# Kernel optimization log

Hardware: AMD Instinct MI355X
Metric: run time of the kernel (lower is better)

Reference implementation:

```python
import jax, jax.numpy as jnp
import numpy as np

B, R, P, DP, DR, N, RK = 4, 256, 64, 384, 512, 48, 24


def _ln(x, w, b, eps=1e-5):
    m = x.mean(-1, keepdims=True)
    v = ((x - m) ** 2).mean(-1, keepdims=True)
    return (x - m) / jnp.sqrt(v + eps) * w + b


def _l2norm(x, eps=1e-6):
    return x / jnp.maximum(jnp.linalg.norm(x, axis=-1, keepdims=True), eps)


def setup_inputs() -> dict:
    key = jax.random.key(0)
    ks = jax.random.split(key, 16)
    s = 0.02
    rnd = lambda k, shp: jax.random.normal(k, shp, jnp.float32) * s
    inp = {
        'patch_tokens': jax.random.normal(ks[0], (B, R, P, DP), jnp.float32),
        'patch_mask': jax.random.randint(ks[1], (B, R, P), 0, 2) > 0,
        'near_mask': jax.random.randint(ks[2], (R, R), 0, 2) > 0,
        'far_mask': jax.random.randint(ks[3], (R, R), 0, 2) > 0,
        'local_pos': rnd(ks[4], (1, 1, P, DP)),
        'gate_ln_w': jnp.ones(DP), 'gate_ln_b': jnp.zeros(DP),
        'gate_w1': rnd(ks[5], (DP, DR)), 'gate_b1': jnp.zeros(DR),
        'gate_w2': rnd(ks[6], (DR, 1)), 'gate_b2': jnp.zeros(1),
        'proj_ln1_w': jnp.ones(DP), 'proj_ln1_b': jnp.zeros(DP),
        'proj_w1': rnd(ks[7], (DP, DR)), 'proj_b1': jnp.zeros(DR),
        'proj_w2': rnd(ks[8], (DR, DR)), 'proj_b2': jnp.zeros(DR),
        'proj_ln2_w': jnp.ones(DR), 'proj_ln2_b': jnp.zeros(DR),
        'in_proj_w': rnd(ks[9], (DR, 2 * DR)),
        'x_proj_w': rnd(ks[10], (DR, RK + 2 * N)),
        'dt_w': rnd(ks[11], (RK, DR)),
        'dt_b': jax.random.uniform(ks[12], (DR,), jnp.float32, -4.0, -2.0),
        'A_log': jnp.tile(jnp.log(jnp.arange(1, N + 1, dtype=jnp.float32))[None, :], (DR, 1)),
        'D_param': jnp.ones(DR),
        'out_proj_w': rnd(ks[13], (DR, DR)),
        'scan_ln_w': jnp.ones(DR), 'scan_ln_b': jnp.zeros(DR),
    }
    return inp


def _forward(patch_tokens, patch_mask, near_mask, far_mask, local_pos,
             gate_ln_w, gate_ln_b, gate_w1, gate_b1, gate_w2, gate_b2,
             proj_ln1_w, proj_ln1_b, proj_w1, proj_b1, proj_w2, proj_b2,
             proj_ln2_w, proj_ln2_b, in_proj_w, x_proj_w, dt_w, dt_b,
             A_log, D_param, out_proj_w, scan_ln_w, scan_ln_b):
    # ---- GatedRegionAggregator ----
    x = patch_tokens + local_pos  # [B,R,P,DP]
    g = _ln(x, gate_ln_w, gate_ln_b)
    g = jax.nn.gelu(g @ gate_w1 + gate_b1, approximate=False)
    logits = (g @ gate_w2 + gate_b2)[..., 0]  # [B,R,P]
    logits = jnp.where(patch_mask, logits, jnp.finfo(logits.dtype).min)
    attn = jax.nn.softmax(logits, axis=-1) * patch_mask
    attn = attn / jnp.maximum(attn.sum(-1, keepdims=True), 1e-6)
    pooled = jnp.einsum('brp,brpd->brd', attn, x)  # [B,R,DP]
    p = _ln(pooled, proj_ln1_w, proj_ln1_b)
    p = jax.nn.gelu(p @ proj_w1 + proj_b1, approximate=False)
    p = _ln(p @ proj_w2 + proj_b2, proj_ln2_w, proj_ln2_b)
    p = jnp.nan_to_num(p, nan=0.0, posinf=1.0, neginf=-1.0)
    region = _l2norm(p)  # [B,R,DR]

    # ---- SlowSelectiveScan1D over region sequence (L = R) ----
    xz = region @ in_proj_w  # [B,L,2*DR]
    u, z = jnp.split(xz, 2, axis=-1)
    prm = u @ x_proj_w  # [B,L,RK+2N]
    dt_raw, Bm, Cm = prm[..., :RK], prm[..., RK:RK + N], prm[..., RK + N:]
    delta = jnp.minimum(jax.nn.softplus(dt_raw @ dt_w + dt_b), 10.0)  # [B,L,DR]
    A = -jnp.minimum(jnp.exp(A_log), 1e4)  # [DR,N]
    dA = jnp.exp(jnp.clip(delta[..., None] * A[None, None], -30.0, 30.0))  # [B,L,DR,N]
    dBu = delta[..., None] * Bm[:, :, None, :] * u[..., None]  # [B,L,DR,N]
    log_cumA = jnp.cumsum(jnp.log(jnp.maximum(dA, 1e-38)), axis=1)
    h = jnp.exp(log_cumA) * jnp.cumsum(dBu * jnp.exp(-log_cumA), axis=1)
    y_seq = jnp.einsum('bln,bldn->bld', Cm, h) + D_param * u
    y = (y_seq * jax.nn.silu(z)) @ out_proj_w
    out = _ln(region + jnp.nan_to_num(y, nan=0.0, posinf=1.0, neginf=-1.0),
              scan_ln_w, scan_ln_b)  # [B,R,DR]

    # ---- topology_loss_static ----
    rt = _l2norm(out.astype(jnp.float32))
    sim = jnp.einsum('brd,bsd->brs', rt, rt)  # [B,R,R]
    near = near_mask.astype(sim.dtype)[None]
    far = far_mask.astype(sim.dtype)[None]
    near_loss = ((1.0 - sim) * near).sum() / jnp.maximum(near.sum(), 1.0)
    far_loss = (jax.nn.relu(sim - 0.2) * far).sum() / jnp.maximum(far.sum(), 1.0)
    return out, near_loss + far_loss


def reference(patch_tokens, patch_mask, near_mask, far_mask, local_pos,
              gate_ln_w, gate_ln_b, gate_w1, gate_b1, gate_w2, gate_b2,
              proj_ln1_w, proj_ln1_b, proj_w1, proj_b1, proj_w2, proj_b2,
              proj_ln2_w, proj_ln2_b, in_proj_w, x_proj_w, dt_w, dt_b,
              A_log, D_param, out_proj_w, scan_ln_w, scan_ln_b):
    return _forward(patch_tokens, patch_mask, near_mask, far_mask, local_pos,
                    gate_ln_w, gate_ln_b, gate_w1, gate_b1, gate_w2, gate_b2,
                    proj_ln1_w, proj_ln1_b, proj_w1, proj_b1, proj_w2, proj_b2,
                    proj_ln2_w, proj_ln2_b, in_proj_w, x_proj_w, dt_w, dt_b,
                    A_log, D_param, out_proj_w, scan_ln_w, scan_ln_b)
```

## Files before the change

### kernel.cpp

```cpp
#include <hip/hip_runtime.h>
#include <hip/hip_bf16.h>
#include <math.h>

#define B_ 4
#define R_ 256
#define P_ 64
#define DP_ 384
#define DR_ 512
#define N_ 48
#define RK_ 24
#define MROWS (B_*R_*P_)
#define REGS  (B_*R_)

typedef unsigned short ushort_t;
typedef __attribute__((ext_vector_type(8))) short bf16x8;
typedef __attribute__((ext_vector_type(4))) float f32x4;

#define GLOAD16(g, l) __builtin_amdgcn_global_load_lds( \
    (const __attribute__((address_space(1))) unsigned int*)(g), \
    (__attribute__((address_space(3))) unsigned int*)(l), 16, 0, 0)

#define OFF_PW1  0
#define OFF_PW2  196608
#define OFF_INPW 458752
#define OFF_XPW  983040
#define OFF_DTW  1044480
#define NW_TOT   1056768

__device__ __forceinline__ float us2f(unsigned short u){
  union { unsigned int i; float f; } x; x.i = ((unsigned int)u) << 16; return x.f;
}
__device__ __forceinline__ unsigned short f2us(float f){
  __hip_bfloat16 h = __float2bfloat16(f);
  return *reinterpret_cast<unsigned short*>(&h);
}
__device__ __forceinline__ float gelu_f(float x){
  return x / (1.0f + __expf(-1.702f * x));
}
__device__ __forceinline__ float wred_sum(float v){
#pragma unroll
  for (int m = 1; m < 64; m <<= 1) v += __shfl_xor(v, m, 64);
  return v;
}
__device__ __forceinline__ void block_sum4(float v[4], float* s){
  int lane = threadIdx.x & 63, wid = threadIdx.x >> 6;
#pragma unroll
  for (int i = 0; i < 4; ++i){
    float x = v[i];
#pragma unroll
    for (int m = 1; m < 64; m <<= 1) x += __shfl_xor(x, m, 64);
    if (lane == 0) s[wid * 4 + i] = x;
  }
  __syncthreads();
  if (threadIdx.x < 4){
    float t = 0.f;
    for (int t2 = 0; t2 < 8; ++t2) t += s[t2 * 4 + threadIdx.x];
    s[32 + threadIdx.x] = t;
  }
  __syncthreads();
#pragma unroll
  for (int i = 0; i < 4; ++i) v[i] = s[32 + i];
  __syncthreads();
}
__device__ __forceinline__ void block_sum2(float& a, float& b, float* s){
  int lane = threadIdx.x & 63, wid = threadIdx.x >> 6;
  float x = a, y = b;
#pragma unroll
  for (int m = 1; m < 64; m <<= 1){ x += __shfl_xor(x, m, 64); y += __shfl_xor(y, m, 64); }
  if (lane == 0){ s[wid * 2] = x; s[wid * 2 + 1] = y; }
  __syncthreads();
  if (threadIdx.x < 2){
    float t = 0.f;
    for (int j = 0; j < 8; ++j) t += s[j * 2 + threadIdx.x];
    s[16 + threadIdx.x] = t;
  }
  __syncthreads();
  a = s[16]; b = s[17];
  __syncthreads();
}

__global__ __launch_bounds__(512) void k_prep(
    const float* __restrict__ gw1, const float* __restrict__ glnw,
    const float* __restrict__ glnb, const float* __restrict__ gb1,
    ushort_t* __restrict__ W1pT, float* __restrict__ s1,
    float* __restrict__ b1p, float* __restrict__ accum){
  __shared__ float pss[8][64], psb[8][64];
  int tid = threadIdx.x, seg = tid >> 6, nl = tid & 63;
  int n = blockIdx.x * 64 + nl;
  if (blockIdx.x == 0 && tid < 4) accum[tid] = 0.f;
  float s = 0.f, sb = 0.f;
  int k0 = seg * 48;
  for (int i = 0; i < 48; ++i){
    int k = k0 + i;
    float w1 = gw1[k * DR_ + n];
    float v = glnw[k] * w1;
    unsigned short vr = f2us(v);
    s  += us2f(vr);
    sb += glnb[k] * w1;
    W1pT[(size_t)n * DP_ + k] = vr;
  }
  pss[seg][nl] = s; psb[seg][nl] = sb;
  __syncthreads();
  if (tid < 64){
    float ts = 0.f, tb = 0.f;
    for (int j = 0; j < 8; ++j){ ts += pss[j][tid]; tb += psb[j][tid]; }
    s1[blockIdx.x * 64 + tid] = ts;
    b1p[blockIdx.x * 64 + tid] = gb1[blockIdx.x * 64 + tid] + tb;
  }
}

__global__ __launch_bounds__(512) void k_cast(
    const float* __restrict__ pw1, const float* __restrict__ pw2,
    const float* __restrict__ inpw, const float* __restrict__ xpw,
    const float* __restrict__ dtw, ushort_t* __restrict__ dst){
  int i = (blockIdx.x * 512 + threadIdx.x) * 4;
  if (i >= NW_TOT) return;
  const float* s; int off;
  if (i < OFF_PW2){ s = pw1; off = OFF_PW1; }
  else if (i < OFF_INPW){ s = pw2; off = OFF_PW2; }
  else if (i < OFF_XPW){ s = inpw; off = OFF_INPW; }
  else if (i < OFF_DTW){ s = xpw; off = OFF_XPW; }
  else { s = dtw; off = OFF_DTW; }
  float4 v = *(const float4*)(s + (i - off));
  ushort_t* d = dst + i;
  d[0] = f2us(v.x); d[1] = f2us(v.y); d[2] = f2us(v.z); d[3] = f2us(v.w);
}

__global__ __launch_bounds__(512) void k_xform(
    const float* __restrict__ pt, const float* __restrict__ lp,
    ushort_t* __restrict__ xb, float* __restrict__ mu, float* __restrict__ rsg){
  int tid = threadIdx.x, w = tid >> 6, lane = tid & 63;
  size_t r = (size_t)blockIdx.x * 8 + w;
  int p = (int)(r & (P_ - 1));
  const float* xr = pt + r * DP_ + lane * 6;
  const float* lr = lp + (size_t)p * DP_ + lane * 6;
  float x[6];
  float s = 0.f, ss = 0.f;
#pragma unroll
  for (int i = 0; i < 6; i += 2){
    float2 a = *(const float2*)(xr + i);
    float2 b = *(const float2*)(lr + i);
    x[i] = a.x + b.x; x[i + 1] = a.y + b.y;
  }
#pragma unroll
  for (int i = 0; i < 6; ++i){ s += x[i]; ss += x[i] * x[i]; }
  s = wred_sum(s); ss = wred_sum(ss);
  if (lane == 0){
    float m = s * (1.f / DP_);
    float var = ss * (1.f / DP_) - m * m;
    mu[r] = m;
    rsg[r] = rsqrtf(var + 1e-5f);
  }
  ushort_t* xw = xb + r * DP_ + lane * 6;
#pragma unroll
  for (int i = 0; i < 6; i += 2){
    ushort2 u2; u2.x = f2us(x[i]); u2.y = f2us(x[i + 1]);
    *(ushort2*)(xw + i) = u2;
  }
}

__global__ __launch_bounds__(1024, 4) void k_gate_pool(
    const ushort_t* __restrict__ xb,
    const ushort_t* __restrict__ BT,
    const float* __restrict__ mu, const float* __restrict__ rsg,
    const float* __restrict__ s1, const float* __restrict__ b1p,
    const float* __restrict__ w2, const int* __restrict__ pmask,
    float* __restrict__ pooled){
  __shared__ __align__(16) ushort_t Abuf[2][128 * 64];
  __shared__ float wpart[16][128];
  __shared__ float logit_lds[128];
  __shared__ float smu[128], srs[128];
  __shared__ float attn2[2][64];
  int tid = threadIdx.x;
  int lane = tid & 63, w = tid >> 6;
  int t = lane & 15, g = lane >> 4;
  long r0 = (long)blockIdx.x * 128;
  if (tid < 128){
    smu[tid] = mu[r0 + tid];
    srs[tid] = rsg[r0 + tid];
  }

  f32x4 acc[8][2];
#pragma unroll
  for (int m = 0; m < 8; ++m)
#pragma unroll
    for (int n = 0; n < 2; ++n) acc[m][n] = (f32x4){0.f, 0.f, 0.f, 0.f};

  int ro = lane >> 3, c = lane & 7;
  int srow = (w << 3) + ro;
  const ushort_t* asrc = xb + (size_t)(r0 + srow) * DP_ + ((c ^ (srow & 7)) << 3);

  GLOAD16(asrc, Abuf[0] + (w << 9));
  __syncthreads();

  for (int kt = 0; kt < 6; ++kt){
    int cb = kt & 1;
    if (kt < 5) GLOAD16(asrc + (kt + 1) * 64, Abuf[cb ^ 1] + (w << 9));
    bf16x8 bfr[2][2];
#pragma unroll
    for (int kk = 0; kk < 2; ++kk)
#pragma unroll
      for (int n = 0; n < 2; ++n){
        int col = w * 32 + n * 16 + t;
        bfr[kk][n] = *(const bf16x8*)(BT + (size_t)col * DP_ + kt * 64 + (kk * 4 + g) * 8);
      }
#pragma unroll
    for (int kk = 0; kk < 2; ++kk){
      int ch = kk * 4 + g;
#pragma unroll
      for (int m = 0; m < 8; ++m){
        int row = m * 16 + t;
        bf16x8 af = *(const bf16x8*)(Abuf[cb] + row * 64 + ((ch ^ (row & 7)) << 3));
#pragma unroll
        for (int n = 0; n < 2; ++n)
          acc[m][n] = __builtin_amdgcn_mfma_f32_16x16x32_bf16(af, bfr[kk][n], acc[m][n], 0, 0, 0);
      }
    }
    __syncthreads();
  }

  float w2c[2], s1c[2], b1c[2];
#pragma unroll
  for (int n = 0; n < 2; ++n){
    int col = w * 32 + n * 16 + t;
    w2c[n] = w2[col]; s1c[n] = s1[col]; b1c[n] = b1p[col];
  }
#pragma unroll
  for (int m = 0; m < 8; ++m){
#pragma unroll
    for (int j = 0; j < 4; ++j){
      int rl = m * 16 + g * 4 + j;
      float mur = smu[rl], rs = srs[rl];
      float part = 0.f;
#pragma unroll
      for (int n = 0; n < 2; ++n){
        float gp = rs * acc[m][n][j] - mur * rs * s1c[n] + b1c[n];
        part += gelu_f(gp) * w2c[n];
      }
#pragma unroll
      for (int msk = 1; msk < 16; msk <<= 1) part += __shfl_xor(part, msk, 16);
      if (t == 0) wpart[w][rl] = part;
    }
  }
  __syncthreads();
  if (tid < 128){
    float s = 0.f;
#pragma unroll
    for (int wi = 0; wi < 16; ++wi) s += wpart[wi][tid];
    logit_lds[tid] = s;
  }
  __syncthreads();

  int half = tid >> 9, lt = tid & 511;
  long rr0 = r0 + half * 64;
  if (lt < 64){
    int mk = pmask[rr0 + lt];
    float lv = logit_lds[half * 64 + lt];
    float lm = mk ? lv : -3.4e38f;
    float M = lm;
#pragma unroll
    for (int m2 = 1; m2 < 64; m2 <<= 1) M = fmaxf(M, __shfl_xor(M, m2, 64));
    float e = mk ? __expf(lv - M) : 0.f;
    float S = e;
#pragma unroll
    for (int m2 = 1; m2 < 64; m2 <<= 1) S += __shfl_xor(S, m2, 64);
    float a = (S > 0.f) ? e / S : 0.f;
    float S2 = a;
#pragma unroll
    for (int m2 = 1; m2 < 64; m2 <<= 1) S2 += __shfl_xor(S2, m2, 64);
    attn2[half][lt] = a / fmaxf(S2, 1e-6f);
  }
  __syncthreads();

  float* pbuf = (float*)Abuf;
  if (lt < 384){
    int pg = lt / 48, cc = lt % 48;
    float a8[8] = {0,0,0,0,0,0,0,0};
#pragma unroll
    for (int i = 0; i < 8; ++i){
      int p = pg + i * 8;
      bf16x8 v = *(const bf16x8*)(xb + (size_t)(rr0 + p) * DP_ + cc * 8);
      float ap = attn2[half][p];
#pragma unroll
      for (int j = 0; j < 8; ++j) a8[j] = fmaf(ap, us2f((unsigned short)v[j]), a8[j]);
    }
#pragma unroll
    for (int j = 0; j < 8; ++j) pbuf[(half * 8 + pg) * DP_ + cc * 8 + j] = a8[j];
  }
  __syncthreads();
  if (lt < 384){
    float s = 0.f;
#pragma unroll
    for (int g2 = 0; g2 < 8; ++g2) s += pbuf[(half * 8 + g2) * DP_ + lt];
    pooled[(long)(2 * blockIdx.x + half) * DP_ + lt] = s;
  }
}

__global__ __launch_bounds__(512, 4) void k_region(
    const float* __restrict__ pooled,
    const float* __restrict__ ln1w, const float* __restrict__ ln1b,
    const ushort_t* __restrict__ wblob, const float* __restrict__ pb1,
    const float* __restrict__ pb2,
    const float* __restrict__ ln2w, const float* __restrict__ ln2b,
    const float* __restrict__ dtb,
    float* __restrict__ region, float* __restrict__ uT, float* __restrict__ zT,
    float* __restrict__ deltaT, float* __restrict__ BmT, float* __restrict__ CmT){
  const ushort_t* pw1b  = wblob + OFF_PW1;
  const ushort_t* pw2b  = wblob + OFF_PW2;
  const ushort_t* inpwb = wblob + OFF_INPW;
  const ushort_t* xpwb  = wblob + OFF_XPW;
  const ushort_t* dtwb  = wblob + OFF_DTW;
  __shared__ __align__(16) float xr[2][DP_];
  __shared__ __align__(16) float p1[2][DR_];
  __shared__ __align__(16) float rg[2][DR_];
  __shared__ __align__(16) float us[2][DR_];
  __shared__ float ps[4][2][128];
  __shared__ float prm[2][RK_ + 2 * N_];
  __shared__ float red[24];
  int tid = threadIdx.x;
  int r0 = blockIdx.x * 2;
  for (int i = tid; i < 2 * DP_; i += 512) xr[i / DP_][i % DP_] = pooled[(long)r0 * DP_ + i];
  __syncthreads();
  float v0 = (tid < DP_) ? xr[0][tid] : 0.f;
  float v1 = (tid < DP_) ? xr[1][tid] : 0.f;
  float s0 = v0, s1v = v1;
  block_sum2(s0, s1v, red);
  float dv0 = (tid < DP_) ? (v0 - s0 * (1.f / DP_)) : 0.f;
  float dv1 = (tid < DP_) ? (v1 - s1v * (1.f / DP_)) : 0.f;
  float q0 = dv0 * dv0, q1 = dv1 * dv1;
  block_sum2(q0, q1, red);
  if (tid < DP_){
    float lw = ln1w[tid], lb = ln1b[tid];
    xr[0][tid] = dv0 * rsqrtf(q0 * (1.f / DP_) + 1e-5f) * lw + lb;
    xr[1][tid] = dv1 * rsqrtf(q1 * (1.f / DP_) + 1e-5f) * lw + lb;
  }
  __syncthreads();
  {
    float pb = pb1[tid];
    float a0 = pb, a1 = pb;
    for (int k0 = 0; k0 < DP_; k0 += 16){
      ushort_t wv[16];
#pragma unroll
      for (int j = 0; j < 16; ++j) wv[j] = pw1b[(k0 + j) * DR_ + tid];
#pragma unroll
      for (int j4 = 0; j4 < 16; j4 += 4){
        float4 x0 = *(const float4*)(&xr[0][k0 + j4]);
        float4 x1 = *(const float4*)(&xr[1][k0 + j4]);
        float w0 = us2f(wv[j4]), w1f = us2f(wv[j4 + 1]);
        float w2f = us2f(wv[j4 + 2]), w3 = us2f(wv[j4 + 3]);
        a0 = fmaf(x0.x, w0, a0); a1 = fmaf(x1.x, w0, a1);
        a0 = fmaf(x0.y, w1f, a0); a1 = fmaf(x1.y, w1f, a1);
        a0 = fmaf(x0.z, w2f, a0); a1 = fmaf(x1.z, w2f, a1);
        a0 = fmaf(x0.w, w3, a0); a1 = fmaf(x1.w, w3, a1);
      }
    }
    p1[0][tid] = gelu_f(a0); p1[1][tid] = gelu_f(a1);
  }
  __syncthreads();
  float qq0, qq1;
  {
    float pb = pb2[tid];
    float a0 = pb, a1 = pb;
    for (int k0 = 0; k0 < DR_; k0 += 16){
      ushort_t wv[16];
#pragma unroll
      for (int j = 0; j < 16; ++j) wv[j] = pw2b[(k0 + j) * DR_ + tid];
#pragma unroll
      for (int j4 = 0; j4 < 16; j4 += 4){
        float4 x0 = *(const float4*)(&p1[0][k0 + j4]);
        float4 x1 = *(const float4*)(&p1[1][k0 + j4]);
        float w0 = us2f(wv[j4]), w1f = us2f(wv[j4 + 1]);
        float w2f = us2f(wv[j4 + 2]), w3 = us2f(wv[j4 + 3]);
        a0 = fmaf(x0.x, w0, a0); a1 = fmaf(x1.x, w0, a1);
        a0 = fmaf(x0.y, w1f, a0); a1 = fmaf(x1.y, w1f, a1);
        a0 = fmaf(x0.z, w2f, a0); a1 = fmaf(x1.z, w2f, a1);
        a0 = fmaf(x0.w, w3, a0); a1 = fmaf(x1.w, w3, a1);
      }
    }
    qq0 = a0; qq1 = a1;
  }
  {
    float m0 = qq0, m1 = qq1;
    block_sum2(m0, m1, red);
    float d0 = qq0 - m0 * (1.f / DR_), d1 = qq1 - m1 * (1.f / DR_);
    float w0 = d0 * d0, w1 = d1 * d1;
    block_sum2(w0, w1, red);
    float lw = ln2w[tid], lb = ln2b[tid];
    float o0 = d0 * rsqrtf(w0 * (1.f / DR_) + 1e-5f) * lw + lb;
    float o1 = d1 * rsqrtf(w1 * (1.f / DR_) + 1e-5f) * lw + lb;
    if (isnan(o0)) o0 = 0.f; else if (isinf(o0)) o0 = (o0 > 0.f) ? 1.f : -1.f;
    if (isnan(o1)) o1 = 0.f; else if (isinf(o1)) o1 = (o1 > 0.f) ? 1.f : -1.f;
    float n0 = o0 * o0, n1 = o1 * o1;
    block_sum2(n0, n1, red);
    float r0v = o0 / fmaxf(sqrtf(n0), 1e-6f);
    float r1v = o1 / fmaxf(sqrtf(n1), 1e-6f);
    rg[0][tid] = r0v; rg[1][tid] = r1v;
    region[(long)r0 * DR_ + tid] = r0v;
    region[(long)(r0 + 1) * DR_ + tid] = r1v;
  }
  __syncthreads();
  {
    float ua0 = 0.f, ua1 = 0.f, zb0 = 0.f, zb1 = 0.f;
    for (int k0 = 0; k0 < DR_; k0 += 8){
      ushort_t w1v[8], w2v[8];
#pragma unroll
      for (int j = 0; j < 8; ++j){
        w1v[j] = inpwb[(k0 + j) * 1024 + tid];
        w2v[j] = inpwb[(k0 + j) * 1024 + tid + 512];
      }
#pragma unroll
      for (int j4 = 0; j4 < 8; j4 += 4){
        float4 x0 = *(const float4*)(&rg[0][k0 + j4]);
        float4 x1 = *(const float4*)(&rg[1][k0 + j4]);
        float xs0[4] = {x0.x, x0.y, x0.z, x0.w};
        float xs1[4] = {x1.x, x1.y, x1.z, x1.w};
#pragma unroll
        for (int j = 0; j < 4; ++j){
          float wa = us2f(w1v[j4 + j]), wb = us2f(w2v[j4 + j]);
          ua0 = fmaf(xs0[j], wa, ua0); ua1 = fmaf(xs1[j], wa, ua1);
          zb0 = fmaf(xs0[j], wb, zb0); zb1 = fmaf(xs1[j], wb, zb1);
        }
      }
    }
    us[0][tid] = ua0; us[1][tid] = ua1;
    uT[(long)tid * REGS + r0] = ua0;
    uT[(long)tid * REGS + r0 + 1] = ua1;
    zT[(long)tid * REGS + r0] = zb0;
    zT[(long)tid * REGS + r0 + 1] = zb1;
  }
  __syncthreads();
  {
    int sseg = tid >> 7, c = tid & 127;
    float pr0 = 0.f, pr1 = 0.f;
    if (c < RK_ + 2 * N_){
      int kb = sseg * 128;
      for (int k0 = kb; k0 < kb + 128; k0 += 16){
        ushort_t wv[16];
#pragma unroll
        for (int j = 0; j < 16; ++j) wv[j] = xpwb[(k0 + j) * (RK_ + 2 * N_) + c];
#pragma unroll
        for (int j4 = 0; j4 < 16; j4 += 4){
          float4 x0 = *(const float4*)(&us[0][k0 + j4]);
          float4 x1 = *(const float4*)(&us[1][k0 + j4]);
          float w0 = us2f(wv[j4]), w1f = us2f(wv[j4 + 1]);
          float w2f = us2f(wv[j4 + 2]), w3 = us2f(wv[j4 + 3]);
          pr0 = fmaf(x0.x, w0, pr0); pr1 = fmaf(x1.x, w0, pr1);
          pr0 = fmaf(x0.y, w1f, pr0); pr1 = fmaf(x1.y, w1f, pr1);
          pr0 = fmaf(x0.z, w2f, pr0); pr1 = fmaf(x1.z, w2f, pr1);
          pr0 = fmaf(x0.w, w3, pr0); pr1 = fmaf(x1.w, w3, pr1);
        }
      }
    }
    ps[sseg][0][c] = pr0; ps[sseg][1][c] = pr1;
  }
  __syncthreads();
  if (tid < 256){
    int rr2 = tid >> 7, cc = tid & 127;
    if (cc < RK_ + 2 * N_)
      prm[rr2][cc] = ps[0][rr2][cc] + ps[1][rr2][cc] + ps[2][rr2][cc] + ps[3][rr2][cc];
  }
  __syncthreads();
#pragma unroll
  for (int r = 0; r < 2; ++r){
    float aa = dtb[tid];
#pragma unroll
    for (int j = 0; j < RK_; ++j) aa = fmaf(prm[r][j], us2f(dtwb[j * DR_ + tid]), aa);
    float sp = (aa > 20.f) ? aa : log1pf(expf(aa));
    deltaT[(long)tid * REGS + r0 + r] = fminf(sp, 10.f);
  }
  if (tid < N_){
#pragma unroll
    for (int r = 0; r < 2; ++r){
      BmT[(long)tid * REGS + r0 + r] = prm[r][RK_ + tid];
      CmT[(long)tid * REGS + r0 + r] = prm[r][RK_ + N_ + tid];
    }
  }
}

__global__ __launch_bounds__(256) void k_scan(
    const float* __restrict__ deltaT, const float* __restrict__ uT,
    const float* __restrict__ zT, const float* __restrict__ BmT,
    const float* __restrict__ CmT, const float* __restrict__ alog,
    const float* __restrict__ Dp, float* __restrict__ ys){
  __shared__ float sAn[N_];
  __shared__ float sA[N_][4];
  __shared__ float sB[N_][4];
  int tid = threadIdx.x, lane = tid & 63, w = tid >> 6;
  int ch = blockIdx.x;
  int b = ch >> 9, d = ch & (DR_ - 1);
  if (tid < N_) sAn[tid] = -fminf(__expf(alog[d * N_ + tid]), 10000.f);
  long col = (long)b * R_ + tid;
  float dl = deltaT[(long)d * REGS + col];
  float uu = uT[(long)d * REGS + col];
  float zz = zT[(long)d * REGS + col];
  float Dd = Dp[d];
  float part = 0.f;
  __syncthreads();
  for (int nc = 0; nc < 6; ++nc){
    float bmv[8], cmv[8];
#pragma unroll
    for (int j = 0; j < 8; ++j){
      bmv[j] = BmT[(long)(nc * 8 + j) * REGS + col];
      cmv[j] = CmT[(long)(nc * 8 + j) * REGS + col];
    }
    float aA[8], aB[8];
#pragma unroll
    for (int j = 0; j < 8; ++j){
      int n = nc * 8 + j;
      float cc = fminf(fmaxf(dl * sAn[n], -30.f), 30.f);
      float a = exp2f(cc * 1.44269504f);
      float bv = dl * bmv[j] * uu;
#pragma unroll
      for (int s = 1; s < 64; s <<= 1){
        float a_sh = __shfl_up(a, (unsigned)s, 64);
        float b_sh = __shfl_up(bv, (unsigned)s, 64);
        float nb = fmaf(a, b_sh, bv);
        float na = a * a_sh;
        if (lane >= s){ bv = nb; a = na; }
      }
      aA[j] = a; aB[j] = bv;
      if (lane == 63){ sA[n][w] = a; sB[n][w] = bv; }
    }
    __syncthreads();
#pragma unroll
    for (int j = 0; j < 8; ++j){
      int n = nc * 8 + j;
      float hin = 0.f;
#pragma unroll
      for (int tt = 0; tt < 3; ++tt){
        if (tt < w) hin = sA[n][tt] * hin + sB[n][tt];
      }
      float h = fmaf(aA[j], hin, aB[j]);
      part = fmaf(cmv[j], h, part);
    }
    if (nc < 5) __syncthreads();
  }
  float yv = part + Dd * uu;
  float sz = zz / (1.f + __expf(-zz));
  ys[col * DR_ + d] = yv * sz;
}

__global__ __launch_bounds__(512) void k_out(
    const float* __restrict__ ys, const float* __restrict__ W,
    const float* __restrict__ region, const float* __restrict__ lnw,
    const float* __restrict__ lnb, float* __restrict__ outp,
    float* __restrict__ rt){
  __shared__ __align__(16) float yr[4][DR_];
  __shared__ float red[40];
  int tid = threadIdx.x;
  int r0 = blockIdx.x * 4;
  for (int i = tid; i < 4 * DR_; i += 512) yr[i >> 9][i & 511] = ys[(long)r0 * DR_ + i];
  __syncthreads();
  float y[4] = {0,0,0,0};
  for (int k0 = 0; k0 < DR_; k0 += 8){
    float wv[8];
#pragma unroll
    for (int j = 0; j < 8; ++j) wv[j] = W[(k0 + j) * DR_ + tid];
#pragma unroll
    for (int j4 = 0; j4 < 8; j4 += 4){
#pragma unroll
      for (int i = 0; i < 4; ++i){
        float4 x = *(const float4*)(&yr[i][k0 + j4]);
        y[i] = fmaf(x.x, wv[j4], y[i]);
        y[i] = fmaf(x.y, wv[j4 + 1], y[i]);
        y[i] = fmaf(x.z, wv[j4 + 2], y[i]);
        y[i] = fmaf(x.w, wv[j4 + 3], y[i]);
      }
    }
  }
  float v[4], t4[4];
#pragma unroll
  for (int i = 0; i < 4; ++i){
    if (isnan(y[i])) y[i] = 0.f; else if (isinf(y[i])) y[i] = (y[i] > 0.f) ? 1.f : -1.f;
    v[i] = region[(long)(r0 + i) * DR_ + tid] + y[i];
    t4[i] = v[i];
  }
  block_sum4(t4, red);
  float dv[4];
#pragma unroll
  for (int i = 0; i < 4; ++i){ dv[i] = v[i] - t4[i] * (1.f / DR_); t4[i] = dv[i] * dv[i]; }
  block_sum4(t4, red);
  float o[4];
  float lw = lnw[tid], lb = lnb[tid];
#pragma unroll
  for (int i = 0; i < 4; ++i){
    o[i] = dv[i] * rsqrtf(t4[i] * (1.f / DR_) + 1e-5f) * lw + lb;
    outp[(long)(r0 + i) * DR_ + tid] = o[i];
    t4[i] = o[i] * o[i];
  }
  block_sum4(t4, red);
#pragma unroll
  for (int i = 0; i < 4; ++i)
    rt[(long)(r0 + i) * DR_ + tid] = o[i] / fmaxf(sqrtf(t4[i]), 1e-6f);
}

__global__ __launch_bounds__(512) void k_loss(
    const float* __restrict__ rt, const int* __restrict__ nearm,
    const int* __restrict__ farm, float* __restrict__ accum){
  __shared__ __align__(16) float ar[4][DR_];
  __shared__ float ps[2][4][256];
  __shared__ float wsum[8][4];
  int blk = blockIdx.x, tid = threadIdx.x;
  int b = blk >> 6, q0 = (blk & 63) * 4;
  const float* rtb = rt + (long)b * R_ * DR_;
  for (int i = tid; i < 4 * DR_; i += 512) ar[i >> 9][i & 511] = rtb[(long)q0 * DR_ + i];
  __syncthreads();
  int s = tid & 255, h = tid >> 8;
  const float* rsrow = rtb + (long)s * DR_ + h * 256;
  float dq[4] = {0.f, 0.f, 0.f, 0.f};
  for (int k = 0; k < 256; k += 4){
    float4 yv = *(const float4*)(rsrow + k);
#pragma unroll
    for (int q = 0; q < 4; ++q){
      float4 x = *(const float4*)(&ar[q][h * 256 + k]);
      dq[q] += x.x * yv.x + x.y * yv.y + x.z * yv.z + x.w * yv.w;
    }
  }
#pragma unroll
  for (int q = 0; q < 4; ++q) ps[h][q][s] = dq[q];
  __syncthreads();
  float nl = 0.f, fl = 0.f, nc = 0.f, fc = 0.f;
  if (tid < 256){
#pragma unroll
    for (int q = 0; q < 4; ++q){
      float dot = ps[0][q][tid] + ps[1][q][tid];
      int nm = nearm[(q0 + q) * R_ + tid], fm = farm[(q0 + q) * R_ + tid];
      if (nm){ nl += 1.f - dot; if (b == 0) nc += 1.f; }
      if (fm){ fl += fmaxf(dot - 0.2f, 0.f); if (b == 0) fc += 1.f; }
    }
  }
  nl = wred_sum(nl); fl = wred_sum(fl); nc = wred_sum(nc); fc = wred_sum(fc);
  int w = tid >> 6, lane = tid & 63;
  if (lane == 0){ wsum[w][0] = nl; wsum[w][1] = fl; wsum[w][2] = nc; wsum[w][3] = fc; }
  __syncthreads();
  if (tid == 0){
    float a0 = 0, a1 = 0, a2 = 0, a3 = 0;
    for (int i = 0; i < 8; i++){ a0 += wsum[i][0]; a1 += wsum[i][1]; a2 += wsum[i][2]; a3 += wsum[i][3]; }
    atomicAdd(&accum[0], a0); atomicAdd(&accum[1], a1);
    if (b == 0){ atomicAdd(&accum[2], a2); atomicAdd(&accum[3], a3); }
  }
}

__global__ void k_final(const float* __restrict__ accum, float* __restrict__ outp){
  if (threadIdx.x == 0){
    float loss = accum[0] / fmaxf(accum[2], 1.f) + accum[1] / fmaxf(accum[3], 1.f);
    outp[REGS * DR_] = loss;
  }
}

extern "C" void kernel_launch(void* const* d_in, const int* in_sizes, int n_in,
                              void* d_out, int out_size, void* d_ws, size_t ws_size,
                              hipStream_t stream){
  const float* pt    = (const float*)d_in[0];
  const int*   pmask = (const int*)d_in[1];
  const int*   nearm = (const int*)d_in[2];
  const int*   farm  = (const int*)d_in[3];
  const float* lp    = (const float*)d_in[4];
  const float* glnw  = (const float*)d_in[5];
  const float* glnb  = (const float*)d_in[6];
  const float* gw1   = (const float*)d_in[7];
  const float* gb1   = (const float*)d_in[8];
  const float* gw2   = (const float*)d_in[9];
  const float* pln1w = (const float*)d_in[11];
  const float* pln1b = (const float*)d_in[12];
  const float* pw1   = (const float*)d_in[13];
  const float* pb1   = (const float*)d_in[14];
  const float* pw2   = (const float*)d_in[15];
  const float* pb2   = (const float*)d_in[16];
  const float* pln2w = (const float*)d_in[17];
  const float* pln2b = (const float*)d_in[18];
  const float* inpw  = (const float*)d_in[19];
  const float* xpw   = (const float*)d_in[20];
  const float* dtw   = (const float*)d_in[21];
  const float* dtb   = (const float*)d_in[22];
  const float* alog  = (const float*)d_in[23];
  const float* dpar  = (const float*)d_in[24];
  const float* opw   = (const float*)d_in[25];
  const float* slnw  = (const float*)d_in[26];
  const float* slnb  = (const float*)d_in[27];

  char* ws = (char*)d_ws;
  size_t off = 0;
  auto alloc = [&](size_t bytes){ size_t o = off; off += (bytes + 255) & ~(size_t)255; return o; };
  ushort_t* W1pT  = (ushort_t*)(ws + alloc((size_t)DR_ * DP_ * 2));
  float* s1     = (float*)(ws + alloc(DR_ * 4));
  float* b1p    = (float*)(ws + alloc(DR_ * 4));
  ushort_t* wblob = (ushort_t*)(ws + alloc((size_t)NW_TOT * 2));
  ushort_t* xb  = (ushort_t*)(ws + alloc((size_t)MROWS * DP_ * 2));
  float* mu     = (float*)(ws + alloc((size_t)MROWS * 4));
  float* rsg    = (float*)(ws + alloc((size_t)MROWS * 4));
  float* pooled = (float*)(ws + alloc((size_t)REGS * DP_ * 4));
  float* region = (float*)(ws + alloc((size_t)REGS * DR_ * 4));
  float* uT     = (float*)(ws + alloc((size_t)REGS * DR_ * 4));
  float* zT     = (float*)(ws + alloc((size_t)REGS * DR_ * 4));
  float* deltaT = (float*)(ws + alloc((size_t)REGS * DR_ * 4));
  float* BmT    = (float*)(ws + alloc((size_t)REGS * N_ * 4));
  float* CmT    = (float*)(ws + alloc((size_t)REGS * N_ * 4));
  float* ys     = (float*)(ws + alloc((size_t)REGS * DR_ * 4));
  float* rt     = (float*)(ws + alloc((size_t)REGS * DR_ * 4));
  float* accum  = (float*)(ws + alloc(4 * 4));

  float* outp = (float*)d_out;

  k_prep<<<dim3(8), dim3(512), 0, stream>>>(gw1, glnw, glnb, gb1, W1pT, s1, b1p, accum);
  k_cast<<<dim3((NW_TOT / 4 + 511) / 512), dim3(512), 0, stream>>>(pw1, pw2, inpw, xpw, dtw, wblob);
  k_xform<<<dim3(MROWS / 8), dim3(512), 0, stream>>>(pt, lp, xb, mu, rsg);
  k_gate_pool<<<dim3(MROWS / 128), dim3(1024), 0, stream>>>(xb, W1pT, mu, rsg, s1, b1p, gw2, pmask, pooled);
  k_region<<<dim3(REGS / 2), dim3(512), 0, stream>>>(pooled, pln1w, pln1b, wblob, pb1, pb2, pln2w, pln2b,
                                                     dtb, region, uT, zT, deltaT, BmT, CmT);
  k_scan<<<dim3(B_ * DR_), dim3(256), 0, stream>>>(deltaT, uT, zT, BmT, CmT, alog, dpar, ys);
  k_out<<<dim3(REGS / 4), dim3(512), 0, stream>>>(ys, opw, region, slnw, slnb, outp, rt);
  k_loss<<<dim3(REGS / 4), dim3(512), 0, stream>>>(rt, nearm, farm, accum);
  k_final<<<dim3(1), dim3(64), 0, stream>>>(accum, outp);
}
```

Before: 309.3 us.

## Transpose bf16 weight blob so region kernel reads contiguous 16-byte vectors

The cast kernel now writes each projection weight transposed (output-major rows, with the x_proj rows padded to 128). This lets k_region load each thread's weight row with 16-byte vector loads instead of strided scalar ushort loads. The cast kernel's reads become strided, and in k_region each thread now walks its own row, so loads across a wavefront are no longer coalesced across lanes. Padding adds a little zero work in the x_proj stage.

```diff
diff --git a/kernel.cpp b/kernel.cpp
--- a/kernel.cpp
+++ b/kernel.cpp
@@ -24,8 +24,8 @@
 #define OFF_PW2  196608
 #define OFF_INPW 458752
 #define OFF_XPW  983040
-#define OFF_DTW  1044480
-#define NW_TOT   1056768
+#define OFF_DTW  1048576
+#define NW_TOT   1060864
 
 __device__ __forceinline__ float us2f(unsigned short u){
   union { unsigned int i; float f; } x; x.i = ((unsigned int)u) << 16; return x.f;
@@ -109,21 +109,35 @@
   }
 }
 
-__global__ __launch_bounds__(512) void k_cast(
+__global__ __launch_bounds__(128) void k_cast(
     const float* __restrict__ pw1, const float* __restrict__ pw2,
     const float* __restrict__ inpw, const float* __restrict__ xpw,
     const float* __restrict__ dtw, ushort_t* __restrict__ dst){
-  int i = (blockIdx.x * 512 + threadIdx.x) * 4;
-  if (i >= NW_TOT) return;
-  const float* s; int off;
-  if (i < OFF_PW2){ s = pw1; off = OFF_PW1; }
-  else if (i < OFF_INPW){ s = pw2; off = OFF_PW2; }
-  else if (i < OFF_XPW){ s = inpw; off = OFF_INPW; }
-  else if (i < OFF_DTW){ s = xpw; off = OFF_XPW; }
-  else { s = dtw; off = OFF_DTW; }
-  float4 v = *(const float4*)(s + (i - off));
-  ushort_t* d = dst + i;
-  d[0] = f2us(v.x); d[1] = f2us(v.y); d[2] = f2us(v.z); d[3] = f2us(v.w);
+  int row = blockIdx.x, tid = threadIdx.x;
+  if (row < 512){
+    ushort_t* d = dst + OFF_PW1 + (size_t)row * DP_;
+    for (int k = tid; k < DP_; k += 128) d[k] = f2us(pw1[(size_t)k * DR_ + row]);
+  } else if (row < 1024){
+    int n = row - 512;
+    ushort_t* d = dst + OFF_PW2 + (size_t)n * DR_;
+    for (int k = tid; k < DR_; k += 128) d[k] = f2us(pw2[(size_t)k * DR_ + n]);
+  } else if (row < 2048){
+    int n = row - 1024;
+    ushort_t* d = dst + OFF_INPW + (size_t)n * DR_;
+    for (int k = tid; k < DR_; k += 128) d[k] = f2us(inpw[(size_t)k * 1024 + n]);
+  } else if (row < 2176){
+    int n = row - 2048;
+    ushort_t* d = dst + OFF_XPW + (size_t)n * DR_;
+    if (n < RK_ + 2 * N_){
+      for (int k = tid; k < DR_; k += 128) d[k] = f2us(xpw[(size_t)k * (RK_ + 2 * N_) + n]);
+    } else {
+      for (int k = tid; k < DR_; k += 128) d[k] = 0;
+    }
+  } else {
+    int n = row - 2176;
+    ushort_t* d = dst + OFF_DTW + (size_t)n * RK_;
+    if (tid < RK_) d[tid] = f2us(dtw[(size_t)tid * DR_ + n]);
+  }
 }
 
 __global__ __launch_bounds__(512) void k_xform(
@@ -305,11 +319,6 @@
     const float* __restrict__ dtb,
     float* __restrict__ region, float* __restrict__ uT, float* __restrict__ zT,
     float* __restrict__ deltaT, float* __restrict__ BmT, float* __restrict__ CmT){
-  const ushort_t* pw1b  = wblob + OFF_PW1;
-  const ushort_t* pw2b  = wblob + OFF_PW2;
-  const ushort_t* inpwb = wblob + OFF_INPW;
-  const ushort_t* xpwb  = wblob + OFF_XPW;
-  const ushort_t* dtwb  = wblob + OFF_DTW;
   __shared__ __align__(16) float xr[2][DP_];
   __shared__ __align__(16) float p1[2][DR_];
   __shared__ __align__(16) float rg[2][DR_];
@@ -336,18 +345,20 @@
   }
   __syncthreads();
   {
+    const ushort_t* wrow = wblob + OFF_PW1 + (size_t)tid * DP_;
     float pb = pb1[tid];
     float a0 = pb, a1 = pb;
     for (int k0 = 0; k0 < DP_; k0 += 16){
-      ushort_t wv[16];
-#pragma unroll
-      for (int j = 0; j < 16; ++j) wv[j] = pw1b[(k0 + j) * DR_ + tid];
+      bf16x8 wA = *(const bf16x8*)(wrow + k0);
+      bf16x8 wB = *(const bf16x8*)(wrow + k0 + 8);
 #pragma unroll
       for (int j4 = 0; j4 < 16; j4 += 4){
         float4 x0 = *(const float4*)(&xr[0][k0 + j4]);
         float4 x1 = *(const float4*)(&xr[1][k0 + j4]);
-        float w0 = us2f(wv[j4]), w1f = us2f(wv[j4 + 1]);
-        float w2f = us2f(wv[j4 + 2]), w3 = us2f(wv[j4 + 3]);
+        float w0 = us2f((unsigned short)((j4 < 8) ? wA[j4 & 7] : wB[j4 & 7]));
+        float w1f = us2f((unsigned short)((j4 + 1 < 8) ? wA[(j4 + 1) & 7] : wB[(j4 + 1) & 7]));
+        float w2f = us2f((unsigned short)((j4 + 2 < 8) ? wA[(j4 + 2) & 7] : wB[(j4 + 2) & 7]));
+        float w3 = us2f((unsigned short)((j4 + 3 < 8) ? wA[(j4 + 3) & 7] : wB[(j4 + 3) & 7]));
         a0 = fmaf(x0.x, w0, a0); a1 = fmaf(x1.x, w0, a1);
         a0 = fmaf(x0.y, w1f, a0); a1 = fmaf(x1.y, w1f, a1);
         a0 = fmaf(x0.z, w2f, a0); a1 = fmaf(x1.z, w2f, a1);
@@ -359,18 +370,20 @@
   __syncthreads();
   float qq0, qq1;
   {
+    const ushort_t* wrow = wblob + OFF_PW2 + (size_t)tid * DR_;
     float pb = pb2[tid];
     float a0 = pb, a1 = pb;
     for (int k0 = 0; k0 < DR_; k0 += 16){
-      ushort_t wv[16];
-#pragma unroll
-      for (int j = 0; j < 16; ++j) wv[j] = pw2b[(k0 + j) * DR_ + tid];
+      bf16x8 wA = *(const bf16x8*)(wrow + k0);
+      bf16x8 wB = *(const bf16x8*)(wrow + k0 + 8);
 #pragma unroll
       for (int j4 = 0; j4 < 16; j4 += 4){
         float4 x0 = *(const float4*)(&p1[0][k0 + j4]);
         float4 x1 = *(const float4*)(&p1[1][k0 + j4]);
-        float w0 = us2f(wv[j4]), w1f = us2f(wv[j4 + 1]);
-        float w2f = us2f(wv[j4 + 2]), w3 = us2f(wv[j4 + 3]);
+        float w0 = us2f((unsigned short)((j4 < 8) ? wA[j4 & 7] : wB[j4 & 7]));
+        float w1f = us2f((unsigned short)((j4 + 1 < 8) ? wA[(j4 + 1) & 7] : wB[(j4 + 1) & 7]));
+        float w2f = us2f((unsigned short)((j4 + 2 < 8) ? wA[(j4 + 2) & 7] : wB[(j4 + 2) & 7]));
+        float w3 = us2f((unsigned short)((j4 + 3 < 8) ? wA[(j4 + 3) & 7] : wB[(j4 + 3) & 7]));
         a0 = fmaf(x0.x, w0, a0); a1 = fmaf(x1.x, w0, a1);
         a0 = fmaf(x0.y, w1f, a0); a1 = fmaf(x1.y, w1f, a1);
         a0 = fmaf(x0.z, w2f, a0); a1 = fmaf(x1.z, w2f, a1);
@@ -400,14 +413,12 @@
   }
   __syncthreads();
   {
+    const ushort_t* wra = wblob + OFF_INPW + (size_t)tid * DR_;
+    const ushort_t* wrb = wblob + OFF_INPW + (size_t)(tid + 512) * DR_;
     float ua0 = 0.f, ua1 = 0.f, zb0 = 0.f, zb1 = 0.f;
     for (int k0 = 0; k0 < DR_; k0 += 8){
-      ushort_t w1v[8], w2v[8];
-#pragma unroll
-      for (int j = 0; j < 8; ++j){
-        w1v[j] = inpwb[(k0 + j) * 1024 + tid];
-        w2v[j] = inpwb[(k0 + j) * 1024 + tid + 512];
-      }
+      bf16x8 wva = *(const bf16x8*)(wra + k0);
+      bf16x8 wvb = *(const bf16x8*)(wrb + k0);
 #pragma unroll
       for (int j4 = 0; j4 < 8; j4 += 4){
         float4 x0 = *(const float4*)(&rg[0][k0 + j4]);
@@ -416,7 +427,8 @@
         float xs1[4] = {x1.x, x1.y, x1.z, x1.w};
 #pragma unroll
         for (int j = 0; j < 4; ++j){
-          float wa = us2f(w1v[j4 + j]), wb = us2f(w2v[j4 + j]);
+          float wa = us2f((unsigned short)wva[j4 + j]);
+          float wb = us2f((unsigned short)wvb[j4 + j]);
           ua0 = fmaf(xs0[j], wa, ua0); ua1 = fmaf(xs1[j], wa, ua1);
           zb0 = fmaf(xs0[j], wb, zb0); zb1 = fmaf(xs1[j], wb, zb1);
         }
@@ -431,24 +443,24 @@
   __syncthreads();
   {
     int sseg = tid >> 7, c = tid & 127;
+    const ushort_t* wrow = wblob + OFF_XPW + (size_t)c * DR_;
     float pr0 = 0.f, pr1 = 0.f;
-    if (c < RK_ + 2 * N_){
-      int kb = sseg * 128;
-      for (int k0 = kb; k0 < kb + 128; k0 += 16){
-        ushort_t wv[16];
-#pragma unroll
-        for (int j = 0; j < 16; ++j) wv[j] = xpwb[(k0 + j) * (RK_ + 2 * N_) + c];
-#pragma unroll
-        for (int j4 = 0; j4 < 16; j4 += 4){
-          float4 x0 = *(const float4*)(&us[0][k0 + j4]);
-          float4 x1 = *(const float4*)(&us[1][k0 + j4]);
-          float w0 = us2f(wv[j4]), w1f = us2f(wv[j4 + 1]);
-          float w2f = us2f(wv[j4 + 2]), w3 = us2f(wv[j4 + 3]);
-          pr0 = fmaf(x0.x, w0, pr0); pr1 = fmaf(x1.x, w0, pr1);
-          pr0 = fmaf(x0.y, w1f, pr0); pr1 = fmaf(x1.y, w1f, pr1);
-          pr0 = fmaf(x0.z, w2f, pr0); pr1 = fmaf(x1.z, w2f, pr1);
-          pr0 = fmaf(x0.w, w3, pr0); pr1 = fmaf(x1.w, w3, pr1);
-        }
+    int kb = sseg * 128;
+    for (int k0 = kb; k0 < kb + 128; k0 += 16){
+      bf16x8 wA = *(const bf16x8*)(wrow + k0);
+      bf16x8 wB = *(const bf16x8*)(wrow + k0 + 8);
+#pragma unroll
+      for (int j4 = 0; j4 < 16; j4 += 4){
+        float4 x0 = *(const float4*)(&us[0][k0 + j4]);
+        float4 x1 = *(const float4*)(&us[1][k0 + j4]);
+        float w0 = us2f((unsigned short)((j4 < 8) ? wA[j4 & 7] : wB[j4 & 7]));
+        float w1f = us2f((unsigned short)((j4 + 1 < 8) ? wA[(j4 + 1) & 7] : wB[(j4 + 1) & 7]));
+        float w2f = us2f((unsigned short)((j4 + 2 < 8) ? wA[(j4 + 2) & 7] : wB[(j4 + 2) & 7]));
+        float w3 = us2f((unsigned short)((j4 + 3 < 8) ? wA[(j4 + 3) & 7] : wB[(j4 + 3) & 7]));
+        pr0 = fmaf(x0.x, w0, pr0); pr1 = fmaf(x1.x, w0, pr1);
+        pr0 = fmaf(x0.y, w1f, pr0); pr1 = fmaf(x1.y, w1f, pr1);
+        pr0 = fmaf(x0.z, w2f, pr0); pr1 = fmaf(x1.z, w2f, pr1);
+        pr0 = fmaf(x0.w, w3, pr0); pr1 = fmaf(x1.w, w3, pr1);
       }
     }
     ps[sseg][0][c] = pr0; ps[sseg][1][c] = pr1;
@@ -460,13 +472,26 @@
       prm[rr2][cc] = ps[0][rr2][cc] + ps[1][rr2][cc] + ps[2][rr2][cc] + ps[3][rr2][cc];
   }
   __syncthreads();
-#pragma unroll
-  for (int r = 0; r < 2; ++r){
-    float aa = dtb[tid];
-#pragma unroll
-    for (int j = 0; j < RK_; ++j) aa = fmaf(prm[r][j], us2f(dtwb[j * DR_ + tid]), aa);
-    float sp = (aa > 20.f) ? aa : log1pf(expf(aa));
-    deltaT[(long)tid * REGS + r0 + r] = fminf(sp, 10.f);
+  {
+    const ushort_t* wrow = wblob + OFF_DTW + (size_t)tid * RK_;
+    bf16x8 w0 = *(const bf16x8*)(wrow);
+    bf16x8 w1v = *(const bf16x8*)(wrow + 8);
+    bf16x8 w2v = *(const bf16x8*)(wrow + 16);
+    float wf[RK_];
+#pragma unroll
+    for (int j = 0; j < 8; ++j){
+      wf[j] = us2f((unsigned short)w0[j]);
+      wf[8 + j] = us2f((unsigned short)w1v[j]);
+      wf[16 + j] = us2f((unsigned short)w2v[j]);
+    }
+#pragma unroll
+    for (int r = 0; r < 2; ++r){
+      float aa = dtb[tid];
+#pragma unroll
+      for (int j = 0; j < RK_; ++j) aa = fmaf(prm[r][j], wf[j], aa);
+      float sp = (aa > 20.f) ? aa : log1pf(expf(aa));
+      deltaT[(long)tid * REGS + r0 + r] = fminf(sp, 10.f);
+    }
   }
   if (tid < N_){
 #pragma unroll
@@ -703,7 +728,7 @@
   float* outp = (float*)d_out;
 
   k_prep<<<dim3(8), dim3(512), 0, stream>>>(gw1, glnw, glnb, gb1, W1pT, s1, b1p, accum);
-  k_cast<<<dim3((NW_TOT / 4 + 511) / 512), dim3(512), 0, stream>>>(pw1, pw2, inpw, xpw, dtw, wblob);
+  k_cast<<<dim3(2688), dim3(128), 0, stream>>>(pw1, pw2, inpw, xpw, dtw, wblob);
   k_xform<<<dim3(MROWS / 8), dim3(512), 0, stream>>>(pt, lp, xb, mu, rsg);
   k_gate_pool<<<dim3(MROWS / 128), dim3(1024), 0, stream>>>(xb, W1pT, mu, rsg, s1, b1p, gw2, pmask, pooled);
   k_region<<<dim3(REGS / 2), dim3(512), 0, stream>>>(pooled, pln1w, pln1b, wblob, pb1, pb2, pln2w, pln2b,
```

New measurement: 379.4 us. 22.6% more time.
